# Performance work log

Measured on AMD Instinct MI355X. Metric: run time of the kernel, lower is better.

Reference implementation:

```python
import jax, jax.numpy as jnp
import numpy as np

B, C, H, W = 8, 64, 160, 160
N_HEADS = 8
EPS = 1e-6


def conv1x1(x, w, b):
    # x: [B, Cin, H, W], w: [Cout, Cin], b: [Cout]
    return jnp.einsum('oc,bchw->bohw', w, x) + b[None, :, None, None]


def setup_inputs() -> dict:
    key = jax.random.key(0)
    ks = jax.random.split(key, 12)
    s = 0.05
    return {
        'high': jax.random.normal(ks[0], (B, C, H, W), jnp.float32),
        'low': jax.random.normal(ks[1], (B, C, H, W), jnp.float32),
        'wq_high': jax.random.normal(ks[2], (C // 2, C), jnp.float32) * s,
        'bq_high': jnp.zeros((C // 2,), jnp.float32),
        'wq_low': jax.random.normal(ks[3], (C // 2, C), jnp.float32) * s,
        'bq_low': jnp.zeros((C // 2,), jnp.float32),
        'wk': jax.random.normal(ks[4], (C, C), jnp.float32) * s,
        'bk': jnp.zeros((C,), jnp.float32),
        'wv': jax.random.normal(ks[5], (C, C), jnp.float32) * s,
        'bv': jnp.zeros((C,), jnp.float32),
        'wo': jax.random.normal(ks[6], (C, C), jnp.float32) * s,
        'bo': jnp.zeros((C,), jnp.float32),
    }


def reference(high, low, wq_high, bq_high, wq_low, bq_low, wk, bk, wv, bv, wo, bo):
    b, c, h, w = low.shape
    p, d, n = N_HEADS, c // N_HEADS, h * w
    # q branches: [B, C//2, H, W] -> [B, P/2, N, d]
    hq = conv1x1(high, wq_high, bq_high).reshape(b, p // 2, d, n).transpose(0, 1, 3, 2)
    lq = conv1x1(low, wq_low, bq_low).reshape(b, p // 2, d, n).transpose(0, 1, 3, 2)
    q = jax.nn.softplus(jnp.concatenate([hq, lq], axis=1))          # [B, P, N, d]
    k = jax.nn.softplus(conv1x1(low, wk, bk).reshape(b, p, d, n))   # [B, P, d, N]
    v = conv1x1(low, wv, bv).reshape(b, p, d, n)                    # [B, P, d, N]
    # linear-attention context: kT v over spatial N
    attn_map = jnp.einsum('bpmn,bpcn->bpmc', k, v)                  # [B, P, d, d]
    norm = 1.0 / jnp.einsum('bpnc,bpc->bpn', q, jnp.sum(k, axis=-1) + EPS)  # [B, P, N]
    out = jnp.einsum('bpnm,bpmc,bpn->bpcn', q, attn_map, norm)      # [B, P, d, N]
    out = out.reshape(b, c, h, w)
    return conv1x1(out, wo, bo)
```

## Files before the change

kernel.cpp:

```cpp
#include <hip/hip_runtime.h>

#define NPIX  25600
#define NB    8
#define NCH   200
#define KPX   128
#define EPSV  1e-6f

#define WS_WQM   0
#define WS_BQM   4096
#define WS_WKVM  4160
#define WS_BKVM  12352
#define WS_KSE   12480
#define WS_PART  12992
#define WS_GM    934592

typedef __attribute__((ext_vector_type(8))) short short8v;
typedef __attribute__((ext_vector_type(4))) float f32x4v;

__device__ __forceinline__ unsigned short f2bf(float x) {
  unsigned u = __float_as_uint(x);
  return (unsigned short)((u + 0x7FFFu + ((u >> 16) & 1u)) >> 16);
}
__device__ __forceinline__ float bf2f(unsigned short h) {
  return __uint_as_float(((unsigned)h) << 16);
}
__device__ __forceinline__ float softplus_(float x) {
  return (x > 20.0f) ? x : __logf(1.0f + __expf(x));
}

__global__ void k0_pack(const float* __restrict__ wq_high, const float* __restrict__ bq_high,
                        const float* __restrict__ wq_low,  const float* __restrict__ bq_low,
                        const float* __restrict__ wk, const float* __restrict__ bk,
                        const float* __restrict__ wv, const float* __restrict__ bv,
                        float* __restrict__ ws) {
  const int tid = threadIdx.x;
  unsigned short* wqm = (unsigned short*)(ws + WS_WQM);
  for (int e = tid; e < 8192; e += 256) {
    int j = e & 7, l = (e >> 3) & 63, frag = e >> 9;
    int sp = frag & 1, ks = (frag >> 1) & 1, mt = frag >> 2;
    int row = mt * 16 + (l & 15), c = ks * 32 + (l >> 4) * 8 + j;
    int head = row >> 3, m = row & 7;
    float v = (head < 4) ? wq_high[(head * 8 + m) * 64 + c]
                         : wq_low[((head - 4) * 8 + m) * 64 + c];
    unsigned short hb = f2bf(v);
    wqm[e] = (sp == 0) ? hb : f2bf(v - bf2f(hb));
  }
  for (int e = tid; e < 64; e += 256) {
    int head = e >> 3, m = e & 7;
    ws[WS_BQM + e] = (head < 4) ? bq_high[head * 8 + m] : bq_low[(head - 4) * 8 + m];
  }
  unsigned short* wmp = (unsigned short*)(ws + WS_WKVM);
  for (int e = tid; e < 16384; e += 256) {
    int j = e & 7, l = (e >> 3) & 63, frag = e >> 9;
    int sp = frag & 1, ks = (frag >> 1) & 1, mt = frag >> 2;
    int row = l & 15, k32 = (l >> 4) * 8 + j, c = ks * 32 + k32;
    int head = (mt & 3) * 2 + (row >> 3), m = row & 7;
    float wv_ = (mt < 4) ? wk[(head * 8 + m) * 64 + c] : wv[(head * 8 + m) * 64 + c];
    unsigned short hb = f2bf(wv_);
    wmp[e] = (sp == 0) ? hb : f2bf(wv_ - bf2f(hb));
  }
  for (int e = tid; e < 128; e += 256) {
    int mt = e >> 4, row = e & 15;
    int head = (mt & 3) * 2 + (row >> 3), m = row & 7;
    ws[WS_BKVM + e] = (mt < 4) ? bk[head * 8 + m] : bv[head * 8 + m];
  }
}

__global__ __attribute__((amdgpu_waves_per_eu(1, 8)))
void k1_kv(const float* __restrict__ low,
           const float* __restrict__ ws,
           float* __restrict__ part) {
  const int b = blockIdx.y, chunk = blockIdx.x;
  const int tid = threadIdx.x, lane = tid & 63;
  const int w = __builtin_amdgcn_readfirstlane(tid >> 6);
  const int l15 = lane & 15, lg = lane >> 4;
  __shared__ float kvL[16384];
  const float* lowb = low + (size_t)b * 64 * NPIX + chunk * KPX + w * 32;
  short8v xhi[2][2], xlo[2][2];
#pragma unroll
  for (int nt = 0; nt < 2; nt++)
#pragma unroll
    for (int ks = 0; ks < 2; ks++) {
      const float* xp = lowb + (size_t)(ks * 32 + lg * 8) * NPIX + nt * 16 + l15;
      float xs[8];
#pragma unroll
      for (int j = 0; j < 8; j++) xs[j] = xp[(size_t)j * NPIX];
#pragma unroll
      for (int j = 0; j < 8; j++) {
        unsigned short h = f2bf(xs[j]);
        xhi[nt][ks][j] = (short)h;
        xlo[nt][ks][j] = (short)f2bf(xs[j] - bf2f(h));
      }
    }
  const unsigned short* wm = (const unsigned short*)(ws + WS_WKVM);
  const float* bm = ws + WS_BKVM;
#pragma unroll
  for (int mt = 0; mt < 8; mt++) {
    f32x4v a0 = {0.f, 0.f, 0.f, 0.f}, a1 = {0.f, 0.f, 0.f, 0.f};
#pragma unroll
    for (int ks = 0; ks < 2; ks++) {
      short8v whi = *(const short8v*)(wm + (((mt * 4 + ks * 2 + 0) * 64) + lane) * 8);
      short8v wlo = *(const short8v*)(wm + (((mt * 4 + ks * 2 + 1) * 64) + lane) * 8);
      a0 = __builtin_amdgcn_mfma_f32_16x16x32_bf16(whi, xhi[0][ks], a0, 0, 0, 0);
      a0 = __builtin_amdgcn_mfma_f32_16x16x32_bf16(whi, xlo[0][ks], a0, 0, 0, 0);
      a0 = __builtin_amdgcn_mfma_f32_16x16x32_bf16(wlo, xhi[0][ks], a0, 0, 0, 0);
      a1 = __builtin_amdgcn_mfma_f32_16x16x32_bf16(whi, xhi[1][ks], a1, 0, 0, 0);
      a1 = __builtin_amdgcn_mfma_f32_16x16x32_bf16(whi, xlo[1][ks], a1, 0, 0, 0);
      a1 = __builtin_amdgcn_mfma_f32_16x16x32_bf16(wlo, xhi[1][ks], a1, 0, 0, 0);
    }
#pragma unroll
    for (int r = 0; r < 4; r++) {
      const int row = mt * 16 + lg * 4 + r;
      const float bb = bm[row];
      float v0 = a0[r] + bb, v1 = a1[r] + bb;
      if (mt < 4) { v0 = softplus_(v0); v1 = softplus_(v1); }
      const int px0 = w * 32 + l15, px1 = w * 32 + 16 + l15;
      kvL[row * 128 + ((((px0 >> 2) ^ (row & 7))) << 2) + (px0 & 3)] = v0;
      kvL[row * 128 + ((((px1 >> 2) ^ (row & 7))) << 2) + (px1 & 3)] = v1;
    }
  }
  __syncthreads();
  const int col = l15;
#pragma unroll
  for (int hh = 0; hh < 2; hh++) {
    const int h = w + hh * 4;
    f32x4v acc = {0.f, 0.f, 0.f, 0.f};
    const int arow = h * 8 + (l15 & 7);
    const int brow = 64 + h * 8 + (col < 8 ? col : 0);
#pragma unroll
    for (int ks = 0; ks < 4; ks++) {
      const int pxl = ks * 32 + lg * 8;
      const int sA = arow & 7;
      float4 af0 = *(const float4*)&kvL[arow * 128 + (((pxl >> 2) ^ sA) << 2)];
      float4 af1 = *(const float4*)&kvL[arow * 128 + ((((pxl >> 2) + 1) ^ sA) << 2)];
      float as[8] = {af0.x, af0.y, af0.z, af0.w, af1.x, af1.y, af1.z, af1.w};
      float bs[8];
      if (col < 8) {
        const int sB = brow & 7;
        float4 bf0 = *(const float4*)&kvL[brow * 128 + (((pxl >> 2) ^ sB) << 2)];
        float4 bf1 = *(const float4*)&kvL[brow * 128 + ((((pxl >> 2) + 1) ^ sB) << 2)];
        bs[0]=bf0.x; bs[1]=bf0.y; bs[2]=bf0.z; bs[3]=bf0.w;
        bs[4]=bf1.x; bs[5]=bf1.y; bs[6]=bf1.z; bs[7]=bf1.w;
      } else {
        const float fill = (col == 8) ? 1.0f : 0.0f;
#pragma unroll
        for (int j = 0; j < 8; j++) bs[j] = fill;
      }
      short8v ahi, alo, bhi, blo;
#pragma unroll
      for (int j = 0; j < 8; j++) {
        unsigned short ha = f2bf(as[j]);
        ahi[j] = (short)ha; alo[j] = (short)f2bf(as[j] - bf2f(ha));
        unsigned short hb = f2bf(bs[j]);
        bhi[j] = (short)hb; blo[j] = (short)f2bf(bs[j] - bf2f(hb));
      }
      acc = __builtin_amdgcn_mfma_f32_16x16x32_bf16(ahi, bhi, acc, 0, 0, 0);
      acc = __builtin_amdgcn_mfma_f32_16x16x32_bf16(ahi, blo, acc, 0, 0, 0);
      acc = __builtin_amdgcn_mfma_f32_16x16x32_bf16(alo, bhi, acc, 0, 0, 0);
    }
    if (lane < 32 && col <= 8) {
      float* pb = part + ((size_t)(b * 8 + h) * NCH + chunk) * 72;
#pragma unroll
      for (int r = 0; r < 4; r++) {
        const int rr = lg * 4 + r;
        if (col < 8) pb[rr * 8 + col] = acc[r];
        else         pb[64 + rr] = acc[r];
      }
    }
  }
}

__global__ void k2_g(const float* __restrict__ part, const float* __restrict__ wo,
                     float* __restrict__ ws) {
  const int b = blockIdx.x >> 3, p = blockIdx.x & 7;
  const int tid = threadIdx.x, lane = tid & 63, sub = tid >> 6;
  __shared__ float red[4][72];
  __shared__ float attnL[72];
  const float* src = part + (size_t)(b * 8 + p) * NCH * 72;
  float s0 = 0.0f, s1 = 0.0f;
  for (int ch = sub * (NCH / 4); ch < (sub + 1) * (NCH / 4); ch++) {
    s0 += src[ch * 72 + lane];
    if (lane < 8) s1 += src[ch * 72 + 64 + lane];
  }
  red[sub][lane] = s0;
  if (lane < 8) red[sub][64 + lane] = s1;
  __syncthreads();
  if (tid < 72) attnL[tid] = (red[0][tid] + red[1][tid]) + (red[2][tid] + red[3][tid]);
  __syncthreads();
  if (tid >= 64) {
    if (tid < 72) ws[WS_KSE + (b * 8 + p) * 8 + (tid - 64)] = attnL[tid] + EPSV;
    return;
  }
  const int o = tid;
  float wrow[8];
#pragma unroll
  for (int c = 0; c < 8; c++) wrow[c] = wo[o * 64 + p * 8 + c];
  unsigned short* gm = (unsigned short*)(ws + WS_GM) + (size_t)b * 8192;
  const int mt2 = o >> 4, lane_ = (p & 3) * 16 + (o & 15), ks = p >> 2;
  short8v hi8, lo8;
#pragma unroll
  for (int m = 0; m < 8; m++) {
    float g = 0.0f;
#pragma unroll
    for (int c = 0; c < 8; c++) g = fmaf(attnL[m * 8 + c], wrow[c], g);
    unsigned short hb = f2bf(g);
    hi8[m] = (short)hb;
    lo8[m] = (short)f2bf(g - bf2f(hb));
  }
  *(short8v*)(gm + (size_t)((mt2 * 4 + ks * 2 + 0) * 64 + lane_) * 8) = hi8;
  *(short8v*)(gm + (size_t)((mt2 * 4 + ks * 2 + 1) * 64 + lane_) * 8) = lo8;
}

__global__ __attribute__((amdgpu_waves_per_eu(1, 8)))
void k3_main(const float* __restrict__ high,
             const float* __restrict__ low,
             const float* __restrict__ ws,
             const float* __restrict__ bo,
             float* __restrict__ out) {
  const int b = blockIdx.y, chunk = blockIdx.x;
  const int tid = threadIdx.x, lane = tid & 63;
  const int w = __builtin_amdgcn_readfirstlane(tid >> 6);
  const int l15 = lane & 15, lg = lane >> 4;
  __shared__ float qL[8192];
  __shared__ float rnL[1024];
  const float* highb = high + (size_t)b * 64 * NPIX + chunk * KPX + w * 32;
  const float* lowb  = low  + (size_t)b * 64 * NPIX + chunk * KPX + w * 32;
  short8v xhi[2][2][2], xlo[2][2][2];
#pragma unroll
  for (int s = 0; s < 2; s++) {
    const float* srcb = (s == 0) ? highb : lowb;
#pragma unroll
    for (int nt = 0; nt < 2; nt++)
#pragma unroll
      for (int ks = 0; ks < 2; ks++) {
        const float* xp = srcb + (size_t)(ks * 32 + lg * 8) * NPIX + nt * 16 + l15;
        float xs[8];
#pragma unroll
        for (int j = 0; j < 8; j++) xs[j] = xp[(size_t)j * NPIX];
#pragma unroll
        for (int j = 0; j < 8; j++) {
          unsigned short h = f2bf(xs[j]);
          xhi[s][nt][ks][j] = (short)h;
          xlo[s][nt][ks][j] = (short)f2bf(xs[j] - bf2f(h));
        }
      }
  }
  const unsigned short* wqm = (const unsigned short*)(ws + WS_WQM);
  const float* bqm = ws + WS_BQM;
#pragma unroll
  for (int mt = 0; mt < 4; mt++) {
    const int s = mt >> 1;
    f32x4v a0 = {0.f, 0.f, 0.f, 0.f}, a1 = {0.f, 0.f, 0.f, 0.f};
#pragma unroll
    for (int ks = 0; ks < 2; ks++) {
      short8v whi = *(const short8v*)(wqm + (((mt * 4 + ks * 2 + 0) * 64) + lane) * 8);
      short8v wlo = *(const short8v*)(wqm + (((mt * 4 + ks * 2 + 1) * 64) + lane) * 8);
      a0 = __builtin_amdgcn_mfma_f32_16x16x32_bf16(whi, xhi[s][0][ks], a0, 0, 0, 0);
      a0 = __builtin_amdgcn_mfma_f32_16x16x32_bf16(whi, xlo[s][0][ks], a0, 0, 0, 0);
      a0 = __builtin_amdgcn_mfma_f32_16x16x32_bf16(wlo, xhi[s][0][ks], a0, 0, 0, 0);
      a1 = __builtin_amdgcn_mfma_f32_16x16x32_bf16(whi, xhi[s][1][ks], a1, 0, 0, 0);
      a1 = __builtin_amdgcn_mfma_f32_16x16x32_bf16(whi, xlo[s][1][ks], a1, 0, 0, 0);
      a1 = __builtin_amdgcn_mfma_f32_16x16x32_bf16(wlo, xhi[s][1][ks], a1, 0, 0, 0);
    }
#pragma unroll
    for (int r = 0; r < 4; r++) {
      const int row = mt * 16 + lg * 4 + r;
      const float bb = bqm[row];
      float v0 = softplus_(a0[r] + bb), v1 = softplus_(a1[r] + bb);
      const int px0 = w * 32 + l15, px1 = w * 32 + 16 + l15;
      qL[row * 128 + ((((px0 >> 2) ^ (row & 7))) << 2) + (px0 & 3)] = v0;
      qL[row * 128 + ((((px1 >> 2) ^ (row & 7))) << 2) + (px1 & 3)] = v1;
    }
  }
  __syncthreads();
  {
    const int px = tid & 127;
    const int hb = (tid >> 7) * 4;
#pragma unroll
    for (int h0 = 0; h0 < 4; h0++) {
      const int h = hb + h0;
      const float* ksep = ws + WS_KSE + (b * 8 + h) * 8;
      float s = 0.0f;
#pragma unroll
      for (int m = 0; m < 8; m++) {
        const int row = h * 8 + m;
        s = fmaf(qL[row * 128 + ((((px >> 2) ^ (row & 7))) << 2) + (px & 3)],
                 ksep[m], s);
      }
      rnL[h * 128 + px] = 1.0f / s;
    }
  }
  __syncthreads();
  const unsigned short* gm = (const unsigned short*)(ws + WS_GM) + (size_t)b * 8192;
#pragma unroll
  for (int nt = 0; nt < 2; nt++) {
    const int px = w * 32 + nt * 16 + l15;
    short8v qhi[2], qlo[2];
#pragma unroll
    for (int ks = 0; ks < 2; ks++) {
      const float rn = rnL[(ks * 4 + lg) * 128 + px];
#pragma unroll
      for (int j = 0; j < 8; j++) {
        const int row = ks * 32 + lg * 8 + j;
        float q = qL[row * 128 + ((((px >> 2) ^ j)) << 2) + (px & 3)] * rn;
        unsigned short h = f2bf(q);
        qhi[ks][j] = (short)h;
        qlo[ks][j] = (short)f2bf(q - bf2f(h));
      }
    }
    f32x4v acc[4];
#pragma unroll
    for (int mt2 = 0; mt2 < 4; mt2++) acc[mt2] = (f32x4v){0.f, 0.f, 0.f, 0.f};
#pragma unroll
    for (int mt2 = 0; mt2 < 4; mt2++) {
#pragma unroll
      for (int ks = 0; ks < 2; ks++) {
        short8v ghi = *(const short8v*)(gm + (size_t)((mt2 * 4 + ks * 2 + 0) * 64 + lane) * 8);
        short8v glo = *(const short8v*)(gm + (size_t)((mt2 * 4 + ks * 2 + 1) * 64 + lane) * 8);
        acc[mt2] = __builtin_amdgcn_mfma_f32_16x16x32_bf16(ghi, qhi[ks], acc[mt2], 0, 0, 0);
        acc[mt2] = __builtin_amdgcn_mfma_f32_16x16x32_bf16(ghi, qlo[ks], acc[mt2], 0, 0, 0);
        acc[mt2] = __builtin_amdgcn_mfma_f32_16x16x32_bf16(glo, qhi[ks], acc[mt2], 0, 0, 0);
      }
    }
    float* ob = out + ((size_t)b * 64) * NPIX + chunk * KPX + px;
#pragma unroll
    for (int mt2 = 0; mt2 < 4; mt2++)
#pragma unroll
      for (int r = 0; r < 4; r++) {
        const int o = mt2 * 16 + lg * 4 + r;
        ob[(size_t)o * NPIX] = acc[mt2][r] + bo[o];
      }
  }
}

extern "C" void kernel_launch(void* const* d_in, const int* in_sizes, int n_in,
                              void* d_out, int out_size, void* d_ws, size_t ws_size,
                              hipStream_t stream) {
  const float* high    = (const float*)d_in[0];
  const float* low     = (const float*)d_in[1];
  const float* wq_high = (const float*)d_in[2];
  const float* bq_high = (const float*)d_in[3];
  const float* wq_low  = (const float*)d_in[4];
  const float* bq_low  = (const float*)d_in[5];
  const float* wk      = (const float*)d_in[6];
  const float* bk      = (const float*)d_in[7];
  const float* wv      = (const float*)d_in[8];
  const float* bv      = (const float*)d_in[9];
  const float* wo      = (const float*)d_in[10];
  const float* bo      = (const float*)d_in[11];
  float* ws  = (float*)d_ws;
  float* out = (float*)d_out;

  k0_pack<<<1, 256, 0, stream>>>(wq_high, bq_high, wq_low, bq_low, wk, bk, wv, bv, ws);
  dim3 grid(NCH, NB);
  k1_kv<<<grid, 256, 0, stream>>>(low, ws, ws + WS_PART);
  k2_g<<<64, 256, 0, stream>>>(ws + WS_PART, wo, ws);
  k3_main<<<grid, 256, 0, stream>>>(high, low, ws, bo, out);
}
```

Before: 112.8 us.

## Process each 128-pixel chunk in two 64-pixel halves to shrink LDS and registers

Both the KV-context kernel and the main output kernel now loop over two 64-pixel halves of each chunk instead of handling all 128 pixels at once. Shared-memory tiles shrink by half, and per-thread register arrays for the input fragments lose a dimension. This is meant to raise occupancy, and the accumulators in k1 persist across the halves. The cost is extra __syncthreads barriers and a serialised load-compute sequence within each block, which may reduce the overlap of memory latency with compute.

```diff
diff --git a/kernel.cpp b/kernel.cpp
--- a/kernel.cpp
+++ b/kernel.cpp
@@ -74,97 +74,98 @@
   const int tid = threadIdx.x, lane = tid & 63;
   const int w = __builtin_amdgcn_readfirstlane(tid >> 6);
   const int l15 = lane & 15, lg = lane >> 4;
-  __shared__ float kvL[16384];
-  const float* lowb = low + (size_t)b * 64 * NPIX + chunk * KPX + w * 32;
-  short8v xhi[2][2], xlo[2][2];
-#pragma unroll
-  for (int nt = 0; nt < 2; nt++)
+  __shared__ float kvL[128 * 64];
+  const float* lowb = low + (size_t)b * 64 * NPIX + chunk * KPX;
+  const unsigned short* wm = (const unsigned short*)(ws + WS_WKVM);
+  const float* bm = ws + WS_BKVM;
+  f32x4v acc[2] = {{0.f,0.f,0.f,0.f},{0.f,0.f,0.f,0.f}};
+  const int col = l15;
+#pragma unroll
+  for (int half = 0; half < 2; half++) {
+    short8v xhi[2], xlo[2];
 #pragma unroll
     for (int ks = 0; ks < 2; ks++) {
-      const float* xp = lowb + (size_t)(ks * 32 + lg * 8) * NPIX + nt * 16 + l15;
+      const float* xp = lowb + (size_t)(ks * 32 + lg * 8) * NPIX + half * 64 + w * 16 + l15;
       float xs[8];
 #pragma unroll
       for (int j = 0; j < 8; j++) xs[j] = xp[(size_t)j * NPIX];
 #pragma unroll
       for (int j = 0; j < 8; j++) {
         unsigned short h = f2bf(xs[j]);
-        xhi[nt][ks][j] = (short)h;
-        xlo[nt][ks][j] = (short)f2bf(xs[j] - bf2f(h));
-      }
-    }
-  const unsigned short* wm = (const unsigned short*)(ws + WS_WKVM);
-  const float* bm = ws + WS_BKVM;
-#pragma unroll
-  for (int mt = 0; mt < 8; mt++) {
-    f32x4v a0 = {0.f, 0.f, 0.f, 0.f}, a1 = {0.f, 0.f, 0.f, 0.f};
-#pragma unroll
-    for (int ks = 0; ks < 2; ks++) {
-      short8v whi = *(const short8v*)(wm + (((mt * 4 + ks * 2 + 0) * 64) + lane) * 8);
-      short8v wlo = *(const short8v*)(wm + (((mt * 4 + ks * 2 + 1) * 64) + lane) * 8);
-      a0 = __builtin_amdgcn_mfma_f32_16x16x32_bf16(whi, xhi[0][ks], a0, 0, 0, 0);
-      a0 = __builtin_amdgcn_mfma_f32_16x16x32_bf16(whi, xlo[0][ks], a0, 0, 0, 0);
-      a0 = __builtin_amdgcn_mfma_f32_16x16x32_bf16(wlo, xhi[0][ks], a0, 0, 0, 0);
-      a1 = __builtin_amdgcn_mfma_f32_16x16x32_bf16(whi, xhi[1][ks], a1, 0, 0, 0);
-      a1 = __builtin_amdgcn_mfma_f32_16x16x32_bf16(whi, xlo[1][ks], a1, 0, 0, 0);
-      a1 = __builtin_amdgcn_mfma_f32_16x16x32_bf16(wlo, xhi[1][ks], a1, 0, 0, 0);
-    }
-#pragma unroll
-    for (int r = 0; r < 4; r++) {
-      const int row = mt * 16 + lg * 4 + r;
-      const float bb = bm[row];
-      float v0 = a0[r] + bb, v1 = a1[r] + bb;
-      if (mt < 4) { v0 = softplus_(v0); v1 = softplus_(v1); }
-      const int px0 = w * 32 + l15, px1 = w * 32 + 16 + l15;
-      kvL[row * 128 + ((((px0 >> 2) ^ (row & 7))) << 2) + (px0 & 3)] = v0;
-      kvL[row * 128 + ((((px1 >> 2) ^ (row & 7))) << 2) + (px1 & 3)] = v1;
-    }
-  }
-  __syncthreads();
-  const int col = l15;
-#pragma unroll
-  for (int hh = 0; hh < 2; hh++) {
-    const int h = w + hh * 4;
-    f32x4v acc = {0.f, 0.f, 0.f, 0.f};
-    const int arow = h * 8 + (l15 & 7);
-    const int brow = 64 + h * 8 + (col < 8 ? col : 0);
-#pragma unroll
-    for (int ks = 0; ks < 4; ks++) {
-      const int pxl = ks * 32 + lg * 8;
-      const int sA = arow & 7;
-      float4 af0 = *(const float4*)&kvL[arow * 128 + (((pxl >> 2) ^ sA) << 2)];
-      float4 af1 = *(const float4*)&kvL[arow * 128 + ((((pxl >> 2) + 1) ^ sA) << 2)];
-      float as[8] = {af0.x, af0.y, af0.z, af0.w, af1.x, af1.y, af1.z, af1.w};
-      float bs[8];
-      if (col < 8) {
-        const int sB = brow & 7;
-        float4 bf0 = *(const float4*)&kvL[brow * 128 + (((pxl >> 2) ^ sB) << 2)];
-        float4 bf1 = *(const float4*)&kvL[brow * 128 + ((((pxl >> 2) + 1) ^ sB) << 2)];
-        bs[0]=bf0.x; bs[1]=bf0.y; bs[2]=bf0.z; bs[3]=bf0.w;
-        bs[4]=bf1.x; bs[5]=bf1.y; bs[6]=bf1.z; bs[7]=bf1.w;
-      } else {
-        const float fill = (col == 8) ? 1.0f : 0.0f;
-#pragma unroll
-        for (int j = 0; j < 8; j++) bs[j] = fill;
-      }
-      short8v ahi, alo, bhi, blo;
-#pragma unroll
-      for (int j = 0; j < 8; j++) {
-        unsigned short ha = f2bf(as[j]);
-        ahi[j] = (short)ha; alo[j] = (short)f2bf(as[j] - bf2f(ha));
-        unsigned short hb = f2bf(bs[j]);
-        bhi[j] = (short)hb; blo[j] = (short)f2bf(bs[j] - bf2f(hb));
-      }
-      acc = __builtin_amdgcn_mfma_f32_16x16x32_bf16(ahi, bhi, acc, 0, 0, 0);
-      acc = __builtin_amdgcn_mfma_f32_16x16x32_bf16(ahi, blo, acc, 0, 0, 0);
-      acc = __builtin_amdgcn_mfma_f32_16x16x32_bf16(alo, bhi, acc, 0, 0, 0);
-    }
-    if (lane < 32 && col <= 8) {
+        xhi[ks][j] = (short)h;
+        xlo[ks][j] = (short)f2bf(xs[j] - bf2f(h));
+      }
+    }
+    if (half) __syncthreads();
+#pragma unroll
+    for (int mt = 0; mt < 8; mt++) {
+      f32x4v a0 = {0.f, 0.f, 0.f, 0.f};
+#pragma unroll
+      for (int ks = 0; ks < 2; ks++) {
+        short8v whi = *(const short8v*)(wm + (((mt * 4 + ks * 2 + 0) * 64) + lane) * 8);
+        short8v wlo = *(const short8v*)(wm + (((mt * 4 + ks * 2 + 1) * 64) + lane) * 8);
+        a0 = __builtin_amdgcn_mfma_f32_16x16x32_bf16(whi, xhi[ks], a0, 0, 0, 0);
+        a0 = __builtin_amdgcn_mfma_f32_16x16x32_bf16(whi, xlo[ks], a0, 0, 0, 0);
+        a0 = __builtin_amdgcn_mfma_f32_16x16x32_bf16(wlo, xhi[ks], a0, 0, 0, 0);
+      }
+#pragma unroll
+      for (int r = 0; r < 4; r++) {
+        const int row = mt * 16 + lg * 4 + r;
+        float v0 = a0[r] + bm[row];
+        if (mt < 4) v0 = softplus_(v0);
+        const int px = w * 16 + l15;
+        kvL[row * 64 + ((((px >> 2) ^ (row & 7))) << 2) + (px & 3)] = v0;
+      }
+    }
+    __syncthreads();
+#pragma unroll
+    for (int hh = 0; hh < 2; hh++) {
+      const int h = w + hh * 4;
+      const int arow = h * 8 + (l15 & 7);
+      const int brow = 64 + h * 8 + (col < 8 ? col : 0);
+#pragma unroll
+      for (int ks2 = 0; ks2 < 2; ks2++) {
+        const int pxl = ks2 * 32 + lg * 8;
+        const int sA = arow & 7;
+        float4 af0 = *(const float4*)&kvL[arow * 64 + (((pxl >> 2) ^ sA) << 2)];
+        float4 af1 = *(const float4*)&kvL[arow * 64 + ((((pxl >> 2) + 1) ^ sA) << 2)];
+        float as[8] = {af0.x, af0.y, af0.z, af0.w, af1.x, af1.y, af1.z, af1.w};
+        float bs[8];
+        if (col < 8) {
+          const int sB = brow & 7;
+          float4 bf0 = *(const float4*)&kvL[brow * 64 + (((pxl >> 2) ^ sB) << 2)];
+          float4 bf1 = *(const float4*)&kvL[brow * 64 + ((((pxl >> 2) + 1) ^ sB) << 2)];
+          bs[0]=bf0.x; bs[1]=bf0.y; bs[2]=bf0.z; bs[3]=bf0.w;
+          bs[4]=bf1.x; bs[5]=bf1.y; bs[6]=bf1.z; bs[7]=bf1.w;
+        } else {
+          const float fill = (col == 8) ? 1.0f : 0.0f;
+#pragma unroll
+          for (int j = 0; j < 8; j++) bs[j] = fill;
+        }
+        short8v ahi, alo, bhi, blo;
+#pragma unroll
+        for (int j = 0; j < 8; j++) {
+          unsigned short ha = f2bf(as[j]);
+          ahi[j] = (short)ha; alo[j] = (short)f2bf(as[j] - bf2f(ha));
+          unsigned short hb = f2bf(bs[j]);
+          bhi[j] = (short)hb; blo[j] = (short)f2bf(bs[j] - bf2f(hb));
+        }
+        acc[hh] = __builtin_amdgcn_mfma_f32_16x16x32_bf16(ahi, bhi, acc[hh], 0, 0, 0);
+        acc[hh] = __builtin_amdgcn_mfma_f32_16x16x32_bf16(ahi, blo, acc[hh], 0, 0, 0);
+        acc[hh] = __builtin_amdgcn_mfma_f32_16x16x32_bf16(alo, bhi, acc[hh], 0, 0, 0);
+      }
+    }
+  }
+  if (lane < 32 && col <= 8) {
+#pragma unroll
+    for (int hh = 0; hh < 2; hh++) {
+      const int h = w + hh * 4;
       float* pb = part + ((size_t)(b * 8 + h) * NCH + chunk) * 72;
 #pragma unroll
       for (int r = 0; r < 4; r++) {
         const int rr = lg * 4 + r;
-        if (col < 8) pb[rr * 8 + col] = acc[r];
-        else         pb[64 + rr] = acc[r];
+        if (col < 8) pb[rr * 8 + col] = acc[hh][r];
+        else         pb[64 + rr] = acc[hh][r];
       }
     }
   }
@@ -221,88 +222,81 @@
   const int tid = threadIdx.x, lane = tid & 63;
   const int w = __builtin_amdgcn_readfirstlane(tid >> 6);
   const int l15 = lane & 15, lg = lane >> 4;
-  __shared__ float qL[8192];
-  __shared__ float rnL[1024];
-  const float* highb = high + (size_t)b * 64 * NPIX + chunk * KPX + w * 32;
-  const float* lowb  = low  + (size_t)b * 64 * NPIX + chunk * KPX + w * 32;
-  short8v xhi[2][2][2], xlo[2][2][2];
-#pragma unroll
-  for (int s = 0; s < 2; s++) {
-    const float* srcb = (s == 0) ? highb : lowb;
-#pragma unroll
-    for (int nt = 0; nt < 2; nt++)
+  __shared__ float qL[64 * 64];
+  __shared__ float rnL[8 * 64];
+  const float* highb = high + (size_t)b * 64 * NPIX + chunk * KPX;
+  const float* lowb  = low  + (size_t)b * 64 * NPIX + chunk * KPX;
+  const unsigned short* wqm = (const unsigned short*)(ws + WS_WQM);
+  const float* bqm = ws + WS_BQM;
+  const unsigned short* gm = (const unsigned short*)(ws + WS_GM) + (size_t)b * 8192;
+#pragma unroll
+  for (int half = 0; half < 2; half++) {
+    short8v xhi[2][2], xlo[2][2];
+#pragma unroll
+    for (int s = 0; s < 2; s++) {
+      const float* srcb = (s == 0) ? highb : lowb;
 #pragma unroll
       for (int ks = 0; ks < 2; ks++) {
-        const float* xp = srcb + (size_t)(ks * 32 + lg * 8) * NPIX + nt * 16 + l15;
+        const float* xp = srcb + (size_t)(ks * 32 + lg * 8) * NPIX + half * 64 + w * 16 + l15;
         float xs[8];
 #pragma unroll
         for (int j = 0; j < 8; j++) xs[j] = xp[(size_t)j * NPIX];
 #pragma unroll
         for (int j = 0; j < 8; j++) {
           unsigned short h = f2bf(xs[j]);
-          xhi[s][nt][ks][j] = (short)h;
-          xlo[s][nt][ks][j] = (short)f2bf(xs[j] - bf2f(h));
+          xhi[s][ks][j] = (short)h;
+          xlo[s][ks][j] = (short)f2bf(xs[j] - bf2f(h));
         }
       }
-  }
-  const unsigned short* wqm = (const unsigned short*)(ws + WS_WQM);
-  const float* bqm = ws + WS_BQM;
-#pragma unroll
-  for (int mt = 0; mt < 4; mt++) {
-    const int s = mt >> 1;
-    f32x4v a0 = {0.f, 0.f, 0.f, 0.f}, a1 = {0.f, 0.f, 0.f, 0.f};
+    }
+    if (half) __syncthreads();
+#pragma unroll
+    for (int mt = 0; mt < 4; mt++) {
+      const int s = mt >> 1;
+      f32x4v a0 = {0.f, 0.f, 0.f, 0.f};
+#pragma unroll
+      for (int ks = 0; ks < 2; ks++) {
+        short8v whi = *(const short8v*)(wqm + (((mt * 4 + ks * 2 + 0) * 64) + lane) * 8);
+        short8v wlo = *(const short8v*)(wqm + (((mt * 4 + ks * 2 + 1) * 64) + lane) * 8);
+        a0 = __builtin_amdgcn_mfma_f32_16x16x32_bf16(whi, xhi[s][ks], a0, 0, 0, 0);
+        a0 = __builtin_amdgcn_mfma_f32_16x16x32_bf16(whi, xlo[s][ks], a0, 0, 0, 0);
+        a0 = __builtin_amdgcn_mfma_f32_16x16x32_bf16(wlo, xhi[s][ks], a0, 0, 0, 0);
+      }
+#pragma unroll
+      for (int r = 0; r < 4; r++) {
+        const int row = mt * 16 + lg * 4 + r;
+        float v0 = softplus_(a0[r] + bqm[row]);
+        const int px = w * 16 + l15;
+        qL[row * 64 + ((((px >> 2) ^ (row & 7))) << 2) + (px & 3)] = v0;
+      }
+    }
+    __syncthreads();
+    {
+      const int px = tid & 63;
+#pragma unroll
+      for (int h0 = 0; h0 < 2; h0++) {
+        const int h = (tid >> 6) * 2 + h0;
+        const float* ksep = ws + WS_KSE + (b * 8 + h) * 8;
+        float s = 0.0f;
+#pragma unroll
+        for (int m = 0; m < 8; m++) {
+          const int row = h * 8 + m;
+          s = fmaf(qL[row * 64 + ((((px >> 2) ^ (row & 7))) << 2) + (px & 3)],
+                   ksep[m], s);
+        }
+        rnL[h * 64 + px] = 1.0f / s;
+      }
+    }
+    __syncthreads();
+    const int px = w * 16 + l15;
+    short8v qhi[2], qlo[2];
 #pragma unroll
     for (int ks = 0; ks < 2; ks++) {
-      short8v whi = *(const short8v*)(wqm + (((mt * 4 + ks * 2 + 0) * 64) + lane) * 8);
-      short8v wlo = *(const short8v*)(wqm + (((mt * 4 + ks * 2 + 1) * 64) + lane) * 8);
-      a0 = __builtin_amdgcn_mfma_f32_16x16x32_bf16(whi, xhi[s][0][ks], a0, 0, 0, 0);
-      a0 = __builtin_amdgcn_mfma_f32_16x16x32_bf16(whi, xlo[s][0][ks], a0, 0, 0, 0);
-      a0 = __builtin_amdgcn_mfma_f32_16x16x32_bf16(wlo, xhi[s][0][ks], a0, 0, 0, 0);
-      a1 = __builtin_amdgcn_mfma_f32_16x16x32_bf16(whi, xhi[s][1][ks], a1, 0, 0, 0);
-      a1 = __builtin_amdgcn_mfma_f32_16x16x32_bf16(whi, xlo[s][1][ks], a1, 0, 0, 0);
-      a1 = __builtin_amdgcn_mfma_f32_16x16x32_bf16(wlo, xhi[s][1][ks], a1, 0, 0, 0);
-    }
-#pragma unroll
-    for (int r = 0; r < 4; r++) {
-      const int row = mt * 16 + lg * 4 + r;
-      const float bb = bqm[row];
-      float v0 = softplus_(a0[r] + bb), v1 = softplus_(a1[r] + bb);
-      const int px0 = w * 32 + l15, px1 = w * 32 + 16 + l15;
-      qL[row * 128 + ((((px0 >> 2) ^ (row & 7))) << 2) + (px0 & 3)] = v0;
-      qL[row * 128 + ((((px1 >> 2) ^ (row & 7))) << 2) + (px1 & 3)] = v1;
-    }
-  }
-  __syncthreads();
-  {
-    const int px = tid & 127;
-    const int hb = (tid >> 7) * 4;
-#pragma unroll
-    for (int h0 = 0; h0 < 4; h0++) {
-      const int h = hb + h0;
-      const float* ksep = ws + WS_KSE + (b * 8 + h) * 8;
-      float s = 0.0f;
-#pragma unroll
-      for (int m = 0; m < 8; m++) {
-        const int row = h * 8 + m;
-        s = fmaf(qL[row * 128 + ((((px >> 2) ^ (row & 7))) << 2) + (px & 3)],
-                 ksep[m], s);
-      }
-      rnL[h * 128 + px] = 1.0f / s;
-    }
-  }
-  __syncthreads();
-  const unsigned short* gm = (const unsigned short*)(ws + WS_GM) + (size_t)b * 8192;
-#pragma unroll
-  for (int nt = 0; nt < 2; nt++) {
-    const int px = w * 32 + nt * 16 + l15;
-    short8v qhi[2], qlo[2];
-#pragma unroll
-    for (int ks = 0; ks < 2; ks++) {
-      const float rn = rnL[(ks * 4 + lg) * 128 + px];
+      const float rn = rnL[(ks * 4 + lg) * 64 + px];
 #pragma unroll
       for (int j = 0; j < 8; j++) {
         const int row = ks * 32 + lg * 8 + j;
-        float q = qL[row * 128 + ((((px >> 2) ^ j)) << 2) + (px & 3)] * rn;
+        float q = qL[row * 64 + ((((px >> 2) ^ j)) << 2) + (px & 3)] * rn;
         unsigned short h = f2bf(q);
         qhi[ks][j] = (short)h;
         qlo[ks][j] = (short)f2bf(q - bf2f(h));
@@ -322,7 +316,7 @@
         acc[mt2] = __builtin_amdgcn_mfma_f32_16x16x32_bf16(glo, qhi[ks], acc[mt2], 0, 0, 0);
       }
     }
-    float* ob = out + ((size_t)b * 64) * NPIX + chunk * KPX + px;
+    float* ob = out + ((size_t)b * 64) * NPIX + chunk * KPX + half * 64 + px;
 #pragma unroll
     for (int mt2 = 0; mt2 < 4; mt2++)
 #pragma unroll
```

After: 269.2 us. 139% more time.
